# Performance work log

Hardware: AMD Instinct MI355X
Metric: run time of the kernel (lower is better)

Reference implementation:

```python
import jax, jax.numpy as jnp
import numpy as np

EPS = 1e-5


def _resize_bilinear_ac(x, h, w):
    # bilinear, align_corners=True; x: [B, C, H, W]
    H, W = x.shape[2], x.shape[3]
    ys = jnp.linspace(0.0, H - 1.0, h)
    xs = jnp.linspace(0.0, W - 1.0, w)
    y0 = jnp.floor(ys).astype(jnp.int32)
    x0 = jnp.floor(xs).astype(jnp.int32)
    y1 = jnp.clip(y0 + 1, 0, H - 1)
    x1 = jnp.clip(x0 + 1, 0, W - 1)
    wy = (ys - y0.astype(ys.dtype))[None, None, :, None]
    wx = (xs - x0.astype(xs.dtype))[None, None, None, :]
    rows0 = x[:, :, y0, :]  # [B,C,h,W]
    rows1 = x[:, :, y1, :]
    a = rows0[:, :, :, x0]
    b = rows0[:, :, :, x1]
    c = rows1[:, :, :, x0]
    d = rows1[:, :, :, x1]
    top = a * (1.0 - wx) + b * wx
    bot = c * (1.0 - wx) + d * wx
    return top * (1.0 - wy) + bot * wy


def _conv3x3(x, w):
    return jax.lax.conv_general_dilated(
        x, w, window_strides=(1, 1), padding=[(1, 1), (1, 1)],
        dimension_numbers=('NCHW', 'OIHW', 'NCHW'))


def _bn(x, g, b, m, v):
    scale = (g / jnp.sqrt(v + EPS))[None, :, None, None]
    shift = (b - m * g / jnp.sqrt(v + EPS))[None, :, None, None]
    return x * scale + shift


def setup_inputs() -> dict:
    key = jax.random.key(0)
    ks = jax.random.split(key, 12)
    B = 8
    xt = jax.random.normal(ks[0], (B, 512, 32, 32), jnp.float32)
    xm = jax.random.normal(ks[1], (B, 512, 64, 64), jnp.float32)
    xl = jax.random.normal(ks[2], (B, 256, 128, 128), jnp.float32)
    alpha = jnp.ones((1,), jnp.float32)
    w0 = jax.random.normal(ks[3], (512, 512, 3, 3), jnp.float32) * 0.02
    g0 = jnp.abs(jax.random.normal(ks[4], (512,), jnp.float32)) * 0.1 + 1.0
    b0 = jax.random.normal(ks[5], (512,), jnp.float32) * 0.1
    m0 = jax.random.normal(ks[6], (512,), jnp.float32) * 0.1
    v0 = jnp.abs(jax.random.normal(ks[7], (512,), jnp.float32)) * 0.1 + 1.0
    w1 = jax.random.normal(ks[8], (256, 512, 3, 3), jnp.float32) * 0.02
    g1 = jnp.abs(jax.random.normal(ks[9], (256,), jnp.float32)) * 0.1 + 1.0
    b1 = jax.random.normal(ks[10], (256,), jnp.float32) * 0.1
    m1 = jax.random.normal(ks[11], (256,), jnp.float32) * 0.1
    v1 = jnp.abs(jax.random.normal(jax.random.fold_in(key, 99), (256,), jnp.float32)) * 0.1 + 1.0
    return {"xt": xt, "xm": xm, "xl": xl, "alpha": alpha,
            "w0": w0, "g0": g0, "b0": b0, "m0": m0, "v0": v0,
            "w1": w1, "g1": g1, "b1": b1, "m1": m1, "v1": v1}


def reference(xt, xm, xl, alpha, w0, g0, b0, m0, v0, w1, g1, b1, m1, v1):
    # DecoderModule.forward: upsample xt to xm size (align_corners=True),
    # fuse with alpha-weighted skip, conv0(512->512,BN,ReLU), conv1(512->256,BN,ReLU).
    # xl is accepted but unused in this forward (as in the source).
    h, w = xm.shape[2], xm.shape[3]
    xup = _resize_bilinear_ac(xt, h, w)
    xfuse = xup + alpha[0] * xm
    x = jax.nn.relu(_bn(_conv3x3(xfuse, w0), g0, b0, m0, v0))
    xt_fea = jax.nn.relu(_bn(_conv3x3(x, w1), g1, b1, m1, v1))
    return xt_fea
```

## Files before the change

kernel.cpp:

```cpp
#include <hip/hip_runtime.h>
#include <stdint.h>

#define EPSV 1e-5f

#define CPLANE 278784

using floatx4 = __attribute__((ext_vector_type(4))) float;
using short8  = __attribute__((ext_vector_type(8))) short;

#define GLD(gp, lp) __builtin_amdgcn_global_load_lds( \
    (const __attribute__((address_space(1))) void*)(gp), \
    (__attribute__((address_space(3))) void*)(lp), 16, 0, 0)

__device__ __forceinline__ unsigned short f2bf(float f) {
  union { float f; unsigned int u; } x; x.f = f;
  unsigned int r = x.u + 0x7fffu + ((x.u >> 16) & 1u);
  return (unsigned short)(r >> 16);
}

__global__ __launch_bounds__(256) void border_zero_kernel(
    unsigned short* __restrict__ Xp0, unsigned short* __restrict__ Xp1) {
  int idx = blockIdx.x * 256 + threadIdx.x;
  int k = idx % 260;
  int rest = idx / 260;
  int cc = rest & 63;
  int b = rest >> 6;
  int py, px;
  if (k < 66)       { py = 0;  px = k; }
  else if (k < 132) { py = 65; px = k - 66; }
  else { int k2 = k - 132; py = 1 + (k2 >> 1); px = (k2 & 1) ? 65 : 0; }
  int off = cc * CPLANE + ((b * 66 + py) * 66 + px) * 8;
  short8 z = {};
  *(short8*)(Xp0 + off) = z;
  *(short8*)(Xp1 + off) = z;
}

__global__ __launch_bounds__(256) void fuse_upsample_kernel(
    const float* __restrict__ xt, const float* __restrict__ xm,
    const float* __restrict__ alpha, unsigned short* __restrict__ Xp) {
  __shared__ float sm[32 * 66];
  __shared__ float st[2 * 32 * 34];

  const int tid = threadIdx.x;
  const int ct = blockIdx.x & 15;
  const int y  = (blockIdx.x >> 4) & 63;
  const int b  = blockIdx.x >> 10;
  const int c0 = ct * 32;

  const float fy = y * (31.0f / 63.0f);
  const int y0 = (int)fy;
  const float wy = fy - (float)y0;
  const int y1 = min(y0 + 1, 31);

  {
    const int cb = (tid >> 6) * 8;
    const int xi = tid & 63;
#pragma unroll
    for (int j = 0; j < 8; ++j) {
      int c = cb + j;
      sm[c * 66 + xi] = xm[(((b << 9) + c0 + c) << 12) + (y << 6) + xi];
    }
  }
#pragma unroll
  for (int j = 0; j < 8; ++j) {
    int idx = j * 256 + tid;
    int xi = idx & 31, cc = (idx >> 5) & 31, h = idx >> 10;
    int yr = h ? y1 : y0;
    st[h * 1088 + cc * 34 + xi] =
        xt[(((b << 9) + c0 + cc) << 10) + (yr << 5) + xi];
  }
  __syncthreads();

  const float a = alpha[0];
  const int xo = tid & 63;
  const int cl = tid >> 6;
  const float fx = xo * (31.0f / 63.0f);
  const int x0 = (int)fx;
  const float wx = fx - (float)x0;
  const int x1 = min(x0 + 1, 31);
  short8 ov;
#pragma unroll
  for (int j = 0; j < 8; ++j) {
    int c = cl * 8 + j;
    float t0 = st[c * 34 + x0], t1 = st[c * 34 + x1];
    float u0 = st[1088 + c * 34 + x0], u1 = st[1088 + c * 34 + x1];
    float top = t0 * (1.0f - wx) + t1 * wx;
    float bot = u0 * (1.0f - wx) + u1 * wx;
    float up = top * (1.0f - wy) + bot * wy;
    float val = up + a * sm[c * 66 + xo];
    ov[j] = (short)f2bf(val);
  }
  *(short8*)(Xp + ((c0 >> 3) + cl) * CPLANE +
             ((b * 66 + y + 1) * 66 + xo + 1) * 8) = ov;
}

template <int COUT>
__global__ __launch_bounds__(256) void prep_w_kernel(
    const float* __restrict__ w, unsigned short* __restrict__ Wg) {
  __shared__ unsigned short l[4608];
  const int o = blockIdx.x, t = threadIdx.x;
  const float* src = w + o * 4608;
#pragma unroll
  for (int j = 0; j < 18; ++j) {
    int idx = j * 256 + t;
    l[(idx % 9) * 512 + idx / 9] = f2bf(src[idx]);
  }
  __syncthreads();
#pragma unroll
  for (int tap = 0; tap < 9; ++tap) {
    int cc = t >> 2;
    int off = ((tap * 64 + cc) * COUT + o) * 8 + ((2 * t) & 7);
    *(unsigned int*)(Wg + off) = *(const unsigned int*)(l + (tap << 9) + 2 * t);
  }
}

template <int COUT, int CTILE, bool FINAL>
__global__ __launch_bounds__(256) void conv3x3_kernel(
    const unsigned short* __restrict__ Xp, const unsigned short* __restrict__ Wg,
    const float* __restrict__ gamma, const float* __restrict__ beta,
    const float* __restrict__ mean, const float* __restrict__ var,
    unsigned short* __restrict__ OutPad, float* __restrict__ OutF) {
  constexpr int NCT = COUT / CTILE;
  constexpr int NI  = CTILE / 32;
  constexpr int NWG = 256 * NCT;
  constexpr int QXC = NWG / 8;
  __shared__ unsigned short Abuf[16896];
  __shared__ unsigned short Bbuf0[CTILE * 64];
  __shared__ unsigned short Bbuf1[CTILE * 64];

  const int tid = threadIdx.x;
  const int bid = (int)blockIdx.x;
  const int logical = (bid & 7) * QXC + (bid >> 3);
  const int ptile = logical & 255;
  const int ctile = logical >> 8;
  const int p0 = ptile * 128;
  const int w = tid >> 6;
  const int lane = tid & 63;

  const int pb = p0 >> 12;
  const int yb = (p0 >> 6) & 63;
  const int arowg = ((pb * 66 + yb) * 66) * 8;

  const int fi = lane & 15;
  const int kc = lane >> 4;
  const int wm = w >> 1, wn = w & 1;
  const int aLane = kc * 2112 + (wm + 1) * 528 + (fi + 1) * 8;
  const int bLane = kc * CTILE * 8 + (wn * (CTILE / 2) + fi) * 8;

  floatx4 acc[4][NI] = {};

  auto stageA = [&](int cg) {
#pragma unroll
    for (int kk = 0; kk < 2; ++kk) {
      const int kc2 = 2 * w + kk;
      const unsigned short* g = Xp + (cg * 8 + kc2) * CPLANE + arowg + lane * 8;
      unsigned short* d = Abuf + kc2 * 2112;
#pragma unroll
      for (int rr = 0; rr < 4; ++rr) {
        GLD(g + rr * 528,      d + rr * 528);
        GLD(g + rr * 528 + 16, d + rr * 528 + 16);
      }
    }
  };
  auto stageB = [&](int tap, int cg, unsigned short* dst) {
#pragma unroll
    for (int kk = 0; kk < 2; ++kk) {
      const int kc2 = 2 * w + kk;
      const unsigned short* g =
          Wg + ((tap * 64 + cg * 8 + kc2) * COUT + ctile * CTILE + lane) * 8;
#pragma unroll
      for (int half = 0; half < CTILE / 64; ++half)
        GLD(g + half * 64 * 8, dst + (kc2 * CTILE + half * 64) * 8);
    }
  };
  auto compute = [&](const unsigned short* Bsel, int dy, int dx) {
#pragma unroll
    for (int t = 0; t < 2; ++t) {
      short8 af[4];
#pragma unroll
      for (int mi = 0; mi < 4; ++mi)
        af[mi] = *(const short8*)(Abuf + aLane + t * 8448 + dy * 528 +
                                  (mi * 16 + dx) * 8);
      short8 bfr[NI];
#pragma unroll
      for (int ni = 0; ni < NI; ++ni)
        bfr[ni] = *(const short8*)(Bsel + bLane + t * CTILE * 32 + ni * 128);
#pragma unroll
      for (int mi = 0; mi < 4; ++mi)
#pragma unroll
        for (int ni = 0; ni < NI; ++ni)
          acc[mi][ni] = __builtin_amdgcn_mfma_f32_16x16x32_bf16(
              af[mi], bfr[ni], acc[mi][ni], 0, 0, 0);
    }
  };

  int buf = 0;
  stageA(0);
  stageB(0, 0, Bbuf0);
  __syncthreads();
  for (int cg = 0; cg < 8; ++cg) {
#pragma unroll
    for (int tap = 0; tap < 9; ++tap) {
      unsigned short* cur = buf ? Bbuf1 : Bbuf0;
      unsigned short* nxt = buf ? Bbuf0 : Bbuf1;
      if (tap < 8)      stageB(tap + 1, cg, nxt);
      else if (cg < 7)  stageB(0, cg + 1, nxt);
      compute(cur, tap / 3 - 1, tap % 3 - 1);
      __syncthreads();
      buf ^= 1;
    }
    if (cg < 7) {
      stageA(cg + 1);
      __syncthreads();
    }
  }

#pragma unroll
  for (int ni = 0; ni < NI; ++ni) {
    const int co = ctile * CTILE + wn * (CTILE / 2) + ni * 16 + fi;
    const float sc = gamma[co] / sqrtf(var[co] + EPSV);
    const float sh2 = beta[co] - mean[co] * sc;
#pragma unroll
    for (int mi = 0; mi < 4; ++mi) {
      const int p = p0 + wm * 64 + mi * 16 + kc * 4;
      const int pbb = p >> 12;
      const int prem = p & 4095;
      if constexpr (FINAL) {
        floatx4 o;
#pragma unroll
        for (int r = 0; r < 4; ++r) o[r] = fmaxf(acc[mi][ni][r] * sc + sh2, 0.0f);
        *(floatx4*)(OutF + ((pbb * COUT + co) << 12) + prem) = o;
      } else {
        const int py = prem >> 6, px = prem & 63;
        unsigned short* dst = OutPad + (co >> 3) * CPLANE +
            ((pbb * 66 + py + 1) * 66 + px + 1) * 8 + (co & 7);
#pragma unroll
        for (int r = 0; r < 4; ++r)
          dst[r * 8] = f2bf(fmaxf(acc[mi][ni][r] * sc + sh2, 0.0f));
      }
    }
  }
}

extern "C" void kernel_launch(void* const* d_in, const int* in_sizes, int n_in,
                              void* d_out, int out_size, void* d_ws, size_t ws_size,
                              hipStream_t stream) {
  const float* xt    = (const float*)d_in[0];
  const float* xm    = (const float*)d_in[1];
  const float* alpha = (const float*)d_in[3];
  const float* w0    = (const float*)d_in[4];
  const float* g0    = (const float*)d_in[5];
  const float* b0    = (const float*)d_in[6];
  const float* m0    = (const float*)d_in[7];
  const float* v0    = (const float*)d_in[8];
  const float* w1    = (const float*)d_in[9];
  const float* g1    = (const float*)d_in[10];
  const float* b1    = (const float*)d_in[11];
  const float* m1    = (const float*)d_in[12];
  const float* v1    = (const float*)d_in[13];
  float* out = (float*)d_out;

  char* ws = (char*)d_ws;
  unsigned short* Xp0 = (unsigned short*)(ws);
  unsigned short* Xp1 = (unsigned short*)(ws + 35684352);
  unsigned short* Wg0 = (unsigned short*)(ws + 2 * 35684352);
  unsigned short* Wg1 = (unsigned short*)(ws + 2 * 35684352 + 4718592);

  border_zero_kernel<<<520, 256, 0, stream>>>(Xp0, Xp1);
  prep_w_kernel<512><<<512, 256, 0, stream>>>(w0, Wg0);
  prep_w_kernel<256><<<256, 256, 0, stream>>>(w1, Wg1);
  fuse_upsample_kernel<<<8192, 256, 0, stream>>>(xt, xm, alpha, Xp0);
  conv3x3_kernel<512, 128, false><<<1024, 256, 0, stream>>>(Xp0, Wg0, g0, b0, m0, v0, Xp1, nullptr);
  conv3x3_kernel<256, 128, true><<<512, 256, 0, stream>>>(Xp1, Wg1, g1, b1, m1, v1, nullptr, out);
}
```

Measured before the change: 461.5 us.

## Use larger 256x256 output tile conv kernel for first convolution

Adds a 512-thread conv kernel computing a 256-pixel by 256-channel tile per block, with each wave holding an 8x4 grid of MFMA accumulators. The A tile is staged once per channel group and reused across all nine taps, while B is double-buffered. This is meant to raise data reuse and cut global/LDS traffic per FLOP for the 512->512 conv. In exchange, the grid shrinks to one block per CU, register pressure is high, and a barrier after every tap with a non-overlapped A load may expose latency.

```diff
diff --git a/kernel.cpp b/kernel.cpp
--- a/kernel.cpp
+++ b/kernel.cpp
@@ -111,6 +111,128 @@
     int cc = t >> 2;
     int off = ((tap * 64 + cc) * COUT + o) * 8 + ((2 * t) & 7);
     *(unsigned int*)(Wg + off) = *(const unsigned int*)(l + (tap << 9) + 2 * t);
+  }
+}
+
+template <int COUT, bool FINAL>
+__global__ __launch_bounds__(512, 2) void conv3x3_fat_kernel(
+    const unsigned short* __restrict__ Xp, const unsigned short* __restrict__ Wg,
+    const float* __restrict__ gamma, const float* __restrict__ beta,
+    const float* __restrict__ mean, const float* __restrict__ var,
+    unsigned short* __restrict__ OutPad, float* __restrict__ OutF) {
+  constexpr int NCT = COUT / 256;
+  constexpr int NWG = 128 * NCT;
+  constexpr int QXC = NWG / 8;
+  constexpr int AKS = 3176;
+  constexpr int BKS = 2056;
+  __shared__ unsigned short Abuf[8 * AKS];
+  __shared__ unsigned short Bbuf0[8 * BKS];
+  __shared__ unsigned short Bbuf1[8 * BKS];
+
+  const int tid = threadIdx.x;
+  const int w = tid >> 6;
+  const int lane = tid & 63;
+  const int wm = w >> 2;
+  const int wn = w & 3;
+  const int fi = lane & 15;
+  const int kc4 = lane >> 4;
+
+  const int bid = (int)blockIdx.x;
+  const int logical = (bid & 7) * QXC + (bid >> 3);
+  const int ptile = logical & 127;
+  const int ctile = logical >> 7;
+  const int p0 = ptile * 256;
+  const int pb = p0 >> 12;
+  const int y0 = (p0 >> 6) & 63;
+  const int arowg = ((pb * 66 + y0) * 66) * 8;
+
+  floatx4 acc[8][4] = {};
+
+  auto stageA = [&](int cg) {
+    const unsigned short* g = Xp + (cg * 8 + w) * CPLANE + arowg + lane * 8;
+    unsigned short* d = Abuf + w * AKS;
+#pragma unroll
+    for (int rr = 0; rr < 6; ++rr) {
+      GLD(g + rr * 528,      d + rr * 528);
+      GLD(g + rr * 528 + 16, d + rr * 528 + 16);
+    }
+  };
+  auto stageB = [&](int tap, int cg, unsigned short* dst) {
+    const unsigned short* g =
+        Wg + ((tap * 64 + cg * 8 + w) * COUT + ctile * 256) * 8 + lane * 8;
+    unsigned short* d = dst + w * BKS;
+#pragma unroll
+    for (int ch = 0; ch < 4; ++ch) GLD(g + ch * 512, d + ch * 512);
+  };
+  auto compute = [&](const unsigned short* Bsel, int dy, int dx) {
+#pragma unroll
+    for (int t = 0; t < 2; ++t) {
+      const unsigned short* ab = Abuf + (kc4 + 4 * t) * AKS;
+      short8 af[8];
+#pragma unroll
+      for (int mi = 0; mi < 8; ++mi)
+        af[mi] = *(const short8*)(ab + (wm * 2 + (mi >> 2) + 1 + dy) * 528 +
+                                  ((mi & 3) * 16 + fi + 1 + dx) * 8);
+      const unsigned short* bb =
+          Bsel + (kc4 + 4 * t) * BKS + (wn * 64 + fi) * 8;
+      short8 bfr[4];
+#pragma unroll
+      for (int ni = 0; ni < 4; ++ni)
+        bfr[ni] = *(const short8*)(bb + ni * 128);
+#pragma unroll
+      for (int mi = 0; mi < 8; ++mi)
+#pragma unroll
+        for (int ni = 0; ni < 4; ++ni)
+          acc[mi][ni] = __builtin_amdgcn_mfma_f32_16x16x32_bf16(
+              af[mi], bfr[ni], acc[mi][ni], 0, 0, 0);
+    }
+  };
+
+  int buf = 0;
+  stageA(0);
+  stageB(0, 0, Bbuf0);
+  __syncthreads();
+  for (int cg = 0; cg < 8; ++cg) {
+#pragma unroll
+    for (int tap = 0; tap < 9; ++tap) {
+      unsigned short* cur = buf ? Bbuf1 : Bbuf0;
+      unsigned short* nxt = buf ? Bbuf0 : Bbuf1;
+      if (tap < 8)      stageB(tap + 1, cg, nxt);
+      else if (cg < 7)  stageB(0, cg + 1, nxt);
+      compute(cur, tap / 3 - 1, tap % 3 - 1);
+      __syncthreads();
+      buf ^= 1;
+    }
+    if (cg < 7) {
+      stageA(cg + 1);
+      __syncthreads();
+    }
+  }
+
+#pragma unroll
+  for (int ni = 0; ni < 4; ++ni) {
+    const int co = ctile * 256 + wn * 64 + ni * 16 + fi;
+    const float sc = gamma[co] / sqrtf(var[co] + EPSV);
+    const float sh2 = beta[co] - mean[co] * sc;
+#pragma unroll
+    for (int mi = 0; mi < 8; ++mi) {
+      const int p = p0 + wm * 128 + mi * 16 + kc4 * 4;
+      const int pbb = p >> 12;
+      const int prem = p & 4095;
+      if constexpr (FINAL) {
+        floatx4 o;
+#pragma unroll
+        for (int r = 0; r < 4; ++r) o[r] = fmaxf(acc[mi][ni][r] * sc + sh2, 0.0f);
+        *(floatx4*)(OutF + ((pbb * COUT + co) << 12) + prem) = o;
+      } else {
+        const int py = prem >> 6, px = prem & 63;
+        unsigned short* dst = OutPad + (co >> 3) * CPLANE +
+            ((pbb * 66 + py + 1) * 66 + px + 1) * 8 + (co & 7);
+#pragma unroll
+        for (int r = 0; r < 4; ++r)
+          dst[r * 8] = f2bf(fmaxf(acc[mi][ni][r] * sc + sh2, 0.0f));
+      }
+    }
   }
 }
 
@@ -270,6 +392,6 @@
   prep_w_kernel<512><<<512, 256, 0, stream>>>(w0, Wg0);
   prep_w_kernel<256><<<256, 256, 0, stream>>>(w1, Wg1);
   fuse_upsample_kernel<<<8192, 256, 0, stream>>>(xt, xm, alpha, Xp0);
-  conv3x3_kernel<512, 128, false><<<1024, 256, 0, stream>>>(Xp0, Wg0, g0, b0, m0, v0, Xp1, nullptr);
+  conv3x3_fat_kernel<512, false><<<256, 512, 0, stream>>>(Xp0, Wg0, g0, b0, m0, v0, Xp1, nullptr);
   conv3x3_kernel<256, 128, true><<<512, 256, 0, stream>>>(Xp1, Wg1, g1, b1, m1, v1, nullptr, out);
 }
```

Result: faster. 450.9 us (-2.3%).
